# Kernel optimization log

Hardware: AMD Instinct MI355X
Metric: run time of the kernel (lower is better)

## Reference

```python
import jax, jax.numpy as jnp
import numpy as np

HEADS = 16
ROPE_BASE = 10000.0


def _rope(x):
    # x: [B, S, D]; rotate interleaved even/odd pairs across full D
    B, S, D = x.shape
    half = D // 2
    inv_freq = 1.0 / (ROPE_BASE ** (jnp.arange(half, dtype=jnp.float32) * 2.0 / D))
    ang = jnp.arange(S, dtype=jnp.float32)[:, None] * inv_freq[None, :]  # [S, half]
    cos, sin = jnp.cos(ang), jnp.sin(ang)
    xp = x.reshape(B, S, half, 2)
    xe, xo = xp[..., 0], xp[..., 1]
    re = xe * cos - xo * sin
    ro = xe * sin + xo * cos
    return jnp.stack([re, ro], axis=-1).reshape(B, S, D)


def setup_inputs() -> dict:
    key = jax.random.key(0)
    ks = jax.random.split(key, 7)
    B, S, D = 2, 2048, 1024
    sc = 1.0 / np.sqrt(D)
    return {
        "queries": jax.random.normal(ks[0], (B, S, D), jnp.float32),
        "keys": jax.random.normal(ks[1], (B, S, D), jnp.float32),
        "values": jax.random.normal(ks[2], (B, S, D), jnp.float32),
        "Wq": jax.random.normal(ks[3], (D, D), jnp.float32) * sc,
        "Wk": jax.random.normal(ks[4], (D, D), jnp.float32) * sc,
        "Wv": jax.random.normal(ks[5], (D, D), jnp.float32) * sc,
        "Wo": jax.random.normal(ks[6], (D, D), jnp.float32) * sc,
    }


def reference(queries, keys, values, Wq, Wk, Wv, Wo):
    B, S, D = queries.shape
    H = HEADS
    dk = D // H
    # bias-free linear projections (torch Linear: x @ W^T)
    q = _rope(queries @ Wq.T)
    k = _rope(keys @ Wk.T)
    v = _rope(values @ Wv.T)
    # split heads: [B, H, S, dk]
    q = q.reshape(B, S, H, dk).transpose(0, 2, 1, 3)
    k = k.reshape(B, S, H, dk).transpose(0, 2, 1, 3)
    v = v.reshape(B, S, H, dk).transpose(0, 2, 1, 3)
    scores = jnp.einsum("bhqd,bhkd->bhqk", q, k) / jnp.sqrt(jnp.float32(dk))
    attn = jax.nn.softmax(scores, axis=-1)
    ctx = jnp.einsum("bhqk,bhkd->bhqd", attn, v)  # [B, H, S, dk]
    z = ctx.transpose(0, 2, 1, 3).reshape(B, S, D)
    return z @ Wo.T
```

## Files before the change

kernel.cpp:

```cpp
#include <hip/hip_runtime.h>
#include <hip/hip_bf16.h>
#include <math.h>


typedef __attribute__((ext_vector_type(8))) short s8v;
typedef __attribute__((ext_vector_type(8))) __bf16 bf16x8;
typedef __attribute__((ext_vector_type(4))) float f32x4;
typedef __attribute__((ext_vector_type(16))) float f32x16;
typedef __attribute__((ext_vector_type(2))) unsigned u32x2;

__device__ inline unsigned short f2bf(float f) {
    unsigned u = __builtin_bit_cast(unsigned, f);
    u += 0x7FFFu + ((u >> 16) & 1u);
    return (unsigned short)(u >> 16);
}

__device__ inline unsigned pk_bf16(float a, float b) {
    __hip_bfloat162 h = __float22bfloat162_rn(float2{a, b});
    unsigned u;
    __builtin_memcpy(&u, &h, 4);
    return u;
}

__device__ inline f32x4 mfma16(s8v a, s8v b, f32x4 c) {
    return __builtin_amdgcn_mfma_f32_16x16x32_bf16(
        __builtin_bit_cast(bf16x8, a), __builtin_bit_cast(bf16x8, b), c, 0, 0, 0);
}

__device__ inline f32x16 mfma32(s8v a, s8v b, f32x16 c) {
    return __builtin_amdgcn_mfma_f32_32x32x16_bf16(
        __builtin_bit_cast(bf16x8, a), __builtin_bit_cast(bf16x8, b), c, 0, 0, 0);
}

struct CvtArgs {
    const float* s[7];
    unsigned short* d[7];
    int n4[7];
};

__global__ __launch_bounds__(256) void cvt_kernel(CvtArgs a) {
    const int which = blockIdx.y;
    const float4* __restrict__ src = (const float4*)a.s[which];
    unsigned short* __restrict__ dst = a.d[which];
    const int n4 = a.n4[which];
    for (int i = blockIdx.x * 256 + threadIdx.x; i < n4; i += gridDim.x * 256) {
        float4 v = src[i];
        uint2 o;
        o.x = pk_bf16(v.x, v.y);
        o.y = pk_bf16(v.z, v.w);
        *(uint2*)(dst + (size_t)i * 4) = o;
    }
}

__global__ __launch_bounds__(256) void rope_table_kernel(float* __restrict__ cosT,
                                                         float* __restrict__ sinT) {
    int i = blockIdx.x * 256 + threadIdx.x;
    int s = i >> 9, d2 = i & 511;
    float inv = exp2f((float)d2 * (-13.287712379549449f / 512.0f));
    float ang = (float)s * inv;
    float sn, cs;
    sincosf(ang, &sn, &cs);
    cosT[i] = cs;
    sinT[i] = sn;
}

struct GemmArgs {
    const unsigned short* A[3];
    const unsigned short* W[3];
    void* C[3];
    const float* cosT;
    const float* sinT;
    float scale[3];
};

template <bool ROPE>
__global__ __launch_bounds__(256) void gemm_bt(GemmArgs g) {
    constexpr int K = 1024, N = 1024;
    const int z = blockIdx.z;
    const unsigned short* __restrict__ A = g.A[z];
    const unsigned short* __restrict__ W = g.W[z];

    const int tid = threadIdx.x;
    const int lane = tid & 63, wid = tid >> 6;
    const int wr = wid >> 1, wc = wid & 1;
    const int row0 = blockIdx.x * 128, col0 = blockIdx.y * 128;
    const int lr = lane & 15, kofs = (lane >> 4) * 8;

    __shared__ __align__(16) unsigned short As[128][72];
    __shared__ __align__(16) unsigned short Ws[128][72];

    f32x4 acc[4][4] = {};

    const int srow = tid >> 3;
    const int schunk = (tid & 7) * 8;

    for (int k0 = 0; k0 < K; k0 += 64) {
        __syncthreads();
#pragma unroll
        for (int i = 0; i < 4; ++i) {
            int r = srow + i * 32;
            *(s8v*)(&As[r][schunk]) =
                *(const s8v*)(A + (size_t)(row0 + r) * K + k0 + schunk);
            *(s8v*)(&Ws[r][schunk]) =
                *(const s8v*)(W + (size_t)(col0 + r) * K + k0 + schunk);
        }
        __syncthreads();

        s8v af[2][4], bf[2][4];
#pragma unroll
        for (int ks = 0; ks < 2; ++ks) {
#pragma unroll
            for (int m = 0; m < 4; ++m)
                af[ks][m] = *(const s8v*)(&As[wr * 64 + m * 16 + lr][ks * 32 + kofs]);
#pragma unroll
            for (int n = 0; n < 4; ++n)
                bf[ks][n] = *(const s8v*)(&Ws[wc * 64 + n * 16 + lr][ks * 32 + kofs]);
        }
#pragma unroll
        for (int m = 0; m < 4; ++m)
#pragma unroll
            for (int n = 0; n < 4; ++n) {
                acc[m][n] = mfma16(af[0][m], bf[0][n], acc[m][n]);
                acc[m][n] = mfma16(af[1][m], bf[1][n], acc[m][n]);
            }
    }

    const int rbase = row0 + wr * 64 + ((lane >> 4) << 2);
    const int cbase = col0 + wc * 64 + lr;
    const float scale = g.scale[z];
#pragma unroll
    for (int m = 0; m < 4; ++m) {
#pragma unroll
        for (int n = 0; n < 4; ++n) {
            const int gc = cbase + n * 16;
#pragma unroll
            for (int r = 0; r < 4; ++r) {
                const int gr = rbase + m * 16 + r;
                float v = acc[m][n][r];
                if constexpr (ROPE) {
                    const int s = gr & 2047;
                    const int d2 = gc >> 1;
                    float cs = g.cosT[s * 512 + d2];
                    float sn = g.sinT[s * 512 + d2];
                    float partner = __shfl_xor(v, 1);
                    v = (v * cs + partner * ((lane & 1) ? sn : -sn)) * scale;
                    ((unsigned short*)g.C[z])[(size_t)gr * N + gc] = f2bf(v);
                } else {
                    ((float*)g.C[z])[(size_t)gr * N + gc] = v;
                }
            }
        }
    }
}

__global__ __launch_bounds__(512, 4) void attn_kernel(
    const unsigned short* __restrict__ Q,
    const unsigned short* __restrict__ Km,
    const unsigned short* __restrict__ Vm,
    unsigned short* __restrict__ ctx) {
    const int tid = threadIdx.x;
    const int lane = tid & 63;
    const int w = tid >> 6;
    const int h = w >> 2;
    const int wp = w & 3;
    const int hi = lane >> 5;
    const int lq = lane & 31;
    const int flat = blockIdx.x;
    const int vid = (flat & 7) * 64 + (flat >> 3);
    const int qt = vid & 15;
    const int bh = vid >> 4;
    const size_t base = (size_t)(bh >> 4) * 2048 * 1024;
    const int hcol = (bh & 15) * 64;
    const int q0 = qt * 128 + wp * 32;
    const int kv0 = h * 1024;

    __shared__ __align__(16) unsigned short Vt[2][64][66];
    __shared__ __align__(16) float comb[4][64][33];

    const int vkey = (tid & 255) >> 3;
    const int vc = tid & 7;

    const unsigned short* kpa = Km + base + (size_t)(kv0 + lq) * 1024 + hcol + hi * 8;
    const unsigned short* kpb = kpa + 32 * 1024;
    const unsigned short* vst = Vm + base + (size_t)(kv0 + vkey) * 1024 + hcol + vc * 8;

    s8v qf[4];
#pragma unroll
    for (int s = 0; s < 4; ++s)
        qf[s] = *(const s8v*)(Q + base + (size_t)(q0 + lq) * 1024 + hcol + s * 16 + hi * 8);

    f32x16 accO0 = {}, accO1 = {};
    float lacc = 0.f;

#if __has_builtin(__builtin_amdgcn_permlane32_swap)
#define PK_SWAP(fi, a0, b0, a1, b1)                                             \
    {                                                                           \
        u32x2 ra_ = __builtin_amdgcn_permlane32_swap((a0), (b0), false, false); \
        u32x2 rb_ = __builtin_amdgcn_permlane32_swap((a1), (b1), false, false); \
        fi.x = (int)ra_[0]; fi.y = (int)rb_[0];                                 \
        fi.z = (int)ra_[1]; fi.w = (int)rb_[1];                                 \
    }
#else
#define PK_SWAP(fi, a0, b0, a1, b1)                                             \
    {                                                                           \
        unsigned own0 = hi ? (b0) : (a0);                                       \
        unsigned own1 = hi ? (b1) : (a1);                                       \
        unsigned snd0 = hi ? (a0) : (b0);                                       \
        unsigned snd1 = hi ? (a1) : (b1);                                       \
        unsigned rcv0 = (unsigned)__shfl_xor((int)snd0, 32);                    \
        unsigned rcv1 = (unsigned)__shfl_xor((int)snd1, 32);                    \
        fi.x = (int)(hi ? rcv0 : own0);                                         \
        fi.y = (int)(hi ? rcv1 : own1);                                         \
        fi.z = (int)(hi ? own0 : rcv0);                                         \
        fi.w = (int)(hi ? own1 : rcv1);                                         \
    }
#endif

    for (int st = 0; st < 16; ++st) {
        s8v v00 = *(const s8v*)vst;
        s8v v01 = *(const s8v*)(vst + 32 * 1024);
        s8v kf[8];
#pragma unroll
        for (int i = 0; i < 8; ++i)
            kf[i] = *(const s8v*)(((i >> 2) ? kpb : kpa) + (i & 3) * 16);
#pragma unroll
        for (int j = 0; j < 8; ++j) {
            Vt[h][vc * 8 + j][vkey] = (unsigned short)v00[j];
            Vt[h][vc * 8 + j][vkey + 32] = (unsigned short)v01[j];
        }
        f32x16 s0 = {}, s1 = {};
        __builtin_amdgcn_s_setprio(1);
#pragma unroll
        for (int s = 0; s < 4; ++s) {
            s0 = mfma32(kf[s], qf[s], s0);
            s1 = mfma32(kf[4 + s], qf[s], s1);
        }
        __builtin_amdgcn_s_setprio(0);
#pragma unroll
        for (int r = 0; r < 16; ++r) {
            s0[r] = exp2f(s0[r]);
            s1[r] = exp2f(s1[r]);
        }
        float t16[16];
#pragma unroll
        for (int r = 0; r < 16; ++r) t16[r] = s0[r] + s1[r];
#pragma unroll
        for (int r = 0; r < 8; ++r) t16[r] += t16[r + 8];
#pragma unroll
        for (int r = 0; r < 4; ++r) t16[r] += t16[r + 4];
        lacc += (t16[0] + t16[1]) + (t16[2] + t16[3]);
        unsigned w0[8], w1[8];
#pragma unroll
        for (int g = 0; g < 4; ++g) {
            const int rr = g * 4;
            w0[g] = pk_bf16(s0[rr], s0[rr + 1]);
            w1[g] = pk_bf16(s0[rr + 2], s0[rr + 3]);
        }
#pragma unroll
        for (int g = 4; g < 8; ++g) {
            const int rr = (g - 4) * 4;
            w0[g] = pk_bf16(s1[rr], s1[rr + 1]);
            w1[g] = pk_bf16(s1[rr + 2], s1[rr + 3]);
        }
        s8v pf[4];
#pragma unroll
        for (int ks = 0; ks < 4; ++ks) {
            int4 fi;
            PK_SWAP(fi, w0[2 * ks], w0[2 * ks + 1], w1[2 * ks], w1[2 * ks + 1]);
            pf[ks] = __builtin_bit_cast(s8v, fi);
        }
        __syncthreads();
        __builtin_amdgcn_s_setprio(1);
#pragma unroll
        for (int ks = 0; ks < 4; ++ks) {
            s8v vf0 = *(const s8v*)&Vt[h][lq][ks * 16 + hi * 8];
            s8v vf1 = *(const s8v*)&Vt[h][32 + lq][ks * 16 + hi * 8];
            accO0 = mfma32(vf0, pf[ks], accO0);
            accO1 = mfma32(vf1, pf[ks], accO1);
        }
        __builtin_amdgcn_s_setprio(0);
        __syncthreads();
        kpa += 65536; kpb += 65536; vst += 65536;
    }
#undef PK_SWAP

    if (h == 1) {
#pragma unroll
        for (int r = 0; r < 16; ++r) {
            comb[wp][lane][r] = accO0[r];
            comb[wp][lane][16 + r] = accO1[r];
        }
        comb[wp][lane][32] = lacc;
    }
    __syncthreads();
    if (h == 0) {
#pragma unroll
        for (int r = 0; r < 16; ++r) {
            accO0[r] += comb[wp][lane][r];
            accO1[r] += comb[wp][lane][16 + r];
        }
        const float l2 = lacc + comb[wp][lane][32];
        const float ltot = l2 + __shfl_xor(l2, 32);
        const float rl = 1.0f / ltot;
        unsigned short* dst = ctx + base + (size_t)(q0 + lq) * 1024 + hcol;
#pragma unroll
        for (int r = 0; r < 16; ++r) {
            const int d = (r & 3) + 8 * (r >> 2) + 4 * hi;
            dst[d] = f2bf(accO0[r] * rl);
            dst[d + 32] = f2bf(accO1[r] * rl);
        }
    }
}

extern "C" void kernel_launch(void* const* d_in, const int* in_sizes, int n_in,
                              void* d_out, int out_size, void* d_ws, size_t ws_size,
                              hipStream_t stream) {
    char* ws = (char*)d_ws;
    size_t off = 0;
    auto alloc = [&](size_t bytes) {
        void* p = ws + off;
        off += (bytes + 255) & ~(size_t)255;
        return p;
    };

    const size_t XB = (size_t)4096 * 1024 * 2;
    const size_t WB = (size_t)1024 * 1024 * 2;
    const size_t TB = (size_t)2048 * 512 * 4;

    unsigned short* Xb[3];
    for (int i = 0; i < 3; ++i) Xb[i] = (unsigned short*)alloc(XB);
    unsigned short* Wb[4];
    for (int i = 0; i < 4; ++i) Wb[i] = (unsigned short*)alloc(WB);
    unsigned short* Qb = (unsigned short*)alloc(XB);
    unsigned short* Kb = (unsigned short*)alloc(XB);
    unsigned short* Vb = (unsigned short*)alloc(XB);
    float* cosT = (float*)alloc(TB);
    float* sinT = (float*)alloc(TB);
    unsigned short* ctx = Xb[0];

    CvtArgs ca;
    unsigned short* dsts[7] = {Xb[0], Xb[1], Xb[2], Wb[0], Wb[1], Wb[2], Wb[3]};
    for (int i = 0; i < 7; ++i) {
        ca.s[i] = (const float*)d_in[i];
        ca.d[i] = dsts[i];
        ca.n4[i] = in_sizes[i] / 4;
    }
    cvt_kernel<<<dim3(1024, 7), 256, 0, stream>>>(ca);

    rope_table_kernel<<<4096, 256, 0, stream>>>(cosT, sinT);

    GemmArgs gp;
    gp.A[0] = Xb[0]; gp.A[1] = Xb[1]; gp.A[2] = Xb[2];
    gp.W[0] = Wb[0]; gp.W[1] = Wb[1]; gp.W[2] = Wb[2];
    gp.C[0] = Qb;    gp.C[1] = Kb;    gp.C[2] = Vb;
    gp.cosT = cosT;  gp.sinT = sinT;
    gp.scale[0] = 0.125f * 1.4426950408889634f;
    gp.scale[1] = 1.0f;
    gp.scale[2] = 1.0f;
    gemm_bt<true><<<dim3(32, 8, 3), 256, 0, stream>>>(gp);

    attn_kernel<<<512, 512, 0, stream>>>(Qb, Kb, Vb, ctx);

    GemmArgs go;
    go.A[0] = ctx;   go.A[1] = ctx;   go.A[2] = ctx;
    go.W[0] = Wb[3]; go.W[1] = Wb[3]; go.W[2] = Wb[3];
    go.C[0] = d_out; go.C[1] = d_out; go.C[2] = d_out;
    go.cosT = cosT;  go.sinT = sinT;
    go.scale[0] = 1.0f; go.scale[1] = 1.0f; go.scale[2] = 1.0f;
    gemm_bt<false><<<dim3(32, 8, 1), 256, 0, stream>>>(go);
}
```

Measured before the change: 162.1 us.

## Stage GEMM tiles via direct global-to-LDS loads with XOR swizzle; smaller output-GEMM tiles

```diff
diff --git a/kernel.cpp b/kernel.cpp
--- a/kernel.cpp
+++ b/kernel.cpp
@@ -31,6 +31,19 @@
     return __builtin_amdgcn_mfma_f32_32x32x16_bf16(
         __builtin_bit_cast(bf16x8, a), __builtin_bit_cast(bf16x8, b), c, 0, 0, 0);
 }
+
+#if __has_builtin(__builtin_amdgcn_global_load_lds)
+#define STAGE16(gsrc, lwavebase)                                                \
+    __builtin_amdgcn_global_load_lds(                                           \
+        (const __attribute__((address_space(1))) unsigned int*)(gsrc),          \
+        (__attribute__((address_space(3))) unsigned int*)(lwavebase), 16, 0, 0)
+#define STAGE_SYNC 1
+#else
+#define STAGE16(gsrc, lwavebase)                                                \
+    { *(s8v*)((unsigned short*)(lwavebase) + (threadIdx.x & 63) * 8) =          \
+          *(const s8v*)(gsrc); }
+#define STAGE_SYNC 0
+#endif
 
 struct CvtArgs {
     const float* s[7];
@@ -57,9 +70,11 @@
     int i = blockIdx.x * 256 + threadIdx.x;
     int s = i >> 9, d2 = i & 511;
     float inv = exp2f((float)d2 * (-13.287712379549449f / 512.0f));
-    float ang = (float)s * inv;
+    float rev = (float)s * inv * 0.15915494309189535f;
+    rev -= floorf(rev);
+    float ang = rev * 6.283185307179586f;
     float sn, cs;
-    sincosf(ang, &sn, &cs);
+    __sincosf(ang, &sn, &cs);
     cosT[i] = cs;
     sinT[i] = sn;
 }
@@ -73,51 +88,60 @@
     float scale[3];
 };
 
-template <bool ROPE>
+template <bool ROPE, int BM>
 __global__ __launch_bounds__(256) void gemm_bt(GemmArgs g) {
     constexpr int K = 1024, N = 1024;
+    constexpr int MR = BM / 32;
+    constexpr int AJ = BM * 8 / 256;
     const int z = blockIdx.z;
     const unsigned short* __restrict__ A = g.A[z];
     const unsigned short* __restrict__ W = g.W[z];
 
     const int tid = threadIdx.x;
-    const int lane = tid & 63, wid = tid >> 6;
-    const int wr = wid >> 1, wc = wid & 1;
-    const int row0 = blockIdx.x * 128, col0 = blockIdx.y * 128;
-    const int lr = lane & 15, kofs = (lane >> 4) * 8;
-
-    __shared__ __align__(16) unsigned short As[128][72];
-    __shared__ __align__(16) unsigned short Ws[128][72];
-
-    f32x4 acc[4][4] = {};
-
-    const int srow = tid >> 3;
-    const int schunk = (tid & 7) * 8;
+    const int lane = tid & 63, wv = tid >> 6;
+    const int wrr = (wv >> 1) * (BM / 2);
+    const int wc = wv & 1;
+    const int row0 = blockIdx.x * BM, col0 = blockIdx.y * 128;
+    const int lr = lane & 15;
+
+    __shared__ __align__(16) unsigned short As[BM][64];
+    __shared__ __align__(16) unsigned short Ws[128][64];
+
+    f32x4 acc[MR][4] = {};
 
     for (int k0 = 0; k0 < K; k0 += 64) {
         __syncthreads();
 #pragma unroll
-        for (int i = 0; i < 4; ++i) {
-            int r = srow + i * 32;
-            *(s8v*)(&As[r][schunk]) =
-                *(const s8v*)(A + (size_t)(row0 + r) * K + k0 + schunk);
-            *(s8v*)(&Ws[r][schunk]) =
-                *(const s8v*)(W + (size_t)(col0 + r) * K + k0 + schunk);
+        for (int j = 0; j < AJ; ++j) {
+            const int cib = j * 256 + wv * 64;
+            const int ci = cib + lane;
+            const int sc = (ci & 7) ^ ((ci >> 3) & 7);
+            STAGE16(A + (size_t)(row0 + (ci >> 3)) * K + k0 + sc * 8,
+                    &As[0][0] + (size_t)cib * 8);
+        }
+#pragma unroll
+        for (int j = 0; j < 4; ++j) {
+            const int cib = j * 256 + wv * 64;
+            const int ci = cib + lane;
+            const int sc = (ci & 7) ^ ((ci >> 3) & 7);
+            STAGE16(W + (size_t)(col0 + (ci >> 3)) * K + k0 + sc * 8,
+                    &Ws[0][0] + (size_t)cib * 8);
         }
         __syncthreads();
 
-        s8v af[2][4], bf[2][4];
+        s8v af[2][MR], bf[2][4];
 #pragma unroll
         for (int ks = 0; ks < 2; ++ks) {
-#pragma unroll
-            for (int m = 0; m < 4; ++m)
-                af[ks][m] = *(const s8v*)(&As[wr * 64 + m * 16 + lr][ks * 32 + kofs]);
+            const int pc = ((ks * 4 + (lane >> 4)) ^ (lr & 7)) * 8;
+#pragma unroll
+            for (int m = 0; m < MR; ++m)
+                af[ks][m] = *(const s8v*)(&As[wrr + m * 16 + lr][pc]);
 #pragma unroll
             for (int n = 0; n < 4; ++n)
-                bf[ks][n] = *(const s8v*)(&Ws[wc * 64 + n * 16 + lr][ks * 32 + kofs]);
-        }
-#pragma unroll
-        for (int m = 0; m < 4; ++m)
+                bf[ks][n] = *(const s8v*)(&Ws[wc * 64 + n * 16 + lr][pc]);
+        }
+#pragma unroll
+        for (int m = 0; m < MR; ++m)
 #pragma unroll
             for (int n = 0; n < 4; ++n) {
                 acc[m][n] = mfma16(af[0][m], bf[0][n], acc[m][n]);
@@ -125,11 +149,11 @@
             }
     }
 
-    const int rbase = row0 + wr * 64 + ((lane >> 4) << 2);
+    const int rbase = row0 + wrr + ((lane >> 4) << 2);
     const int cbase = col0 + wc * 64 + lr;
     const float scale = g.scale[z];
 #pragma unroll
-    for (int m = 0; m < 4; ++m) {
+    for (int m = 0; m < MR; ++m) {
 #pragma unroll
         for (int n = 0; n < 4; ++n) {
             const int gc = cbase + n * 16;
@@ -357,7 +381,7 @@
     gp.scale[0] = 0.125f * 1.4426950408889634f;
     gp.scale[1] = 1.0f;
     gp.scale[2] = 1.0f;
-    gemm_bt<true><<<dim3(32, 8, 3), 256, 0, stream>>>(gp);
+    gemm_bt<true, 128><<<dim3(32, 8, 3), 256, 0, stream>>>(gp);
 
     attn_kernel<<<512, 512, 0, stream>>>(Qb, Kb, Vb, ctx);
 
@@ -367,5 +391,5 @@
     go.C[0] = d_out; go.C[1] = d_out; go.C[2] = d_out;
     go.cosT = cosT;  go.sinT = sinT;
     go.scale[0] = 1.0f; go.scale[1] = 1.0f; go.scale[2] = 1.0f;
-    gemm_bt<false><<<dim3(32, 8, 1), 256, 0, stream>>>(go);
-}
+    gemm_bt<false, 64><<<dim3(64, 8, 1), 256, 0, stream>>>(go);
+}
```

Measured after the change: 156.0 us. -3.8%, faster.
